# Performance work log

Hardware: AMD Instinct MI355X
Metric: run time of the kernel (lower is better)

Reference implementation:

```python
import jax, jax.numpy as jnp
import numpy as np

POPULATION = 1000000.0  # __init__ arg of MarkovChainRNN_Model
B, T, F = 16384, 2048, 2  # batch, timesteps, (beta, gamma) per step


def setup_inputs() -> dict:
    key = jax.random.key(0)
    k1, k2 = jax.random.split(key)
    # per-step (beta, gamma) rates in [0, 1)
    inputs = jax.random.uniform(k1, (B, T, F), dtype=jnp.float32)
    # initial [S, I, R] state; scaled so S+I+R is O(population)
    initial_state = jax.random.uniform(k2, (B, 3), dtype=jnp.float32) * POPULATION
    return {"inputs": inputs, "initial_state": initial_state}


def reference(inputs, initial_state):
    # SIR cell update, one step per day:
    #   new_inf = beta * S * I / N ; new_rec = gamma * I
    #   S' = S - new_inf ; I' = I + new_inf - new_rec ; R' = R + new_rec
    # Keras RNN(cell, return_state=True) -> (last_output, last_state);
    # for an SIR cell output == state, so both returns are the final state.
    def step(state, u):
        beta, gamma = u[:, 0], u[:, 1]            # [B], [B]
        S, I, R = state[:, 0], state[:, 1], state[:, 2]
        new_inf = beta * S * I / POPULATION
        new_rec = gamma * I
        new_state = jnp.stack([S - new_inf,
                               I + new_inf - new_rec,
                               R + new_rec], axis=-1)  # [B, 3]
        return new_state, None

    xs = jnp.transpose(inputs, (1, 0, 2))  # time-major [T, B, F]
    final_state, _ = jax.lax.scan(step, initial_state, xs)
    return (final_state, final_state)
```

## Files before the change

### kernel.cpp

```cpp
#include <hip/hip_runtime.h>
#include <stdint.h>
#include <stddef.h>
#include <math.h>


#define T_STEPS 2048
#define C_STEPS 64
#define NCHUNK  (T_STEPS / C_STEPS)
#define BPB     64
#define PAIRS   (C_STEPS / 2)
#define IPC     32

#define INV_POP 1e-6f

__device__ __forceinline__ void stage_chunk(const float* __restrict__ in,
                                            float4* lds, int b0, int c, int lane)
{
    const int hi = lane >> 5;
    const int q  = lane & 31;
#pragma unroll
    for (int j = 0; j < IPC; ++j) {
        const int bi = 2 * j + hi;
        const int p  = q ^ (bi & 15);
        const float* g = in
            + (size_t)(b0 + bi) * (T_STEPS * 2)
            + (size_t)c * (C_STEPS * 2)
            + (size_t)(p * 4);
        float4* l = lds + j * 64;
        __builtin_amdgcn_global_load_lds(
            (__attribute__((address_space(1))) void*)g,
            (__attribute__((address_space(3))) void*)l,
            16, 0, 0);
    }
}

__device__ __forceinline__ void compute_chunk(const float4* lds, int tid,
                                              float& S, float& I, float& rsum)
{
    const int swz = tid & 15;
    const float4* row = lds + tid * PAIRS;
#pragma unroll
    for (int p = 0; p < PAIRS; ++p) {
        const float4 v = row[p ^ swz];

        float u  = v.x * INV_POP;
        float t1 = u * S;
        float t2 = u * I;
        float w  = fmaf(-v.y, I, I);
        rsum     = fmaf(v.y, I, rsum);
        I = fmaf(I, t1, w);
        S = fmaf(-t2, S, S);

        u  = v.z * INV_POP;
        t1 = u * S;
        t2 = u * I;
        w  = fmaf(-v.w, I, I);
        rsum = fmaf(v.w, I, rsum);
        I = fmaf(I, t1, w);
        S = fmaf(-t2, S, S);
    }
}

#define BAR()    asm volatile("s_barrier" ::: "memory")
#define WAIT32() asm volatile("s_waitcnt vmcnt(32)" ::: "memory")
#define WAIT0()  asm volatile("s_waitcnt vmcnt(0)"  ::: "memory")

__global__ __launch_bounds__(128)
void sir_scan_kernel(const float* __restrict__ in, const float* __restrict__ init,
                     float* __restrict__ out, int half)
{
    __shared__ float4 buf0[BPB * PAIRS];
    __shared__ float4 buf1[BPB * PAIRS];
    __shared__ float4 buf2[BPB * PAIRS];
    __shared__ float4 buf3[BPB * PAIRS];

    const int tid = threadIdx.x;
    const int b0  = blockIdx.x * BPB;

    if (tid < 64) {
        const int gb = b0 + tid;
        float S  = init[gb * 3 + 0];
        float I  = init[gb * 3 + 1];
        float R0 = init[gb * 3 + 2];
        float rsum = 0.0f;

#pragma unroll 1
        for (int c = 0; c < NCHUNK; c += 4) {
            BAR(); compute_chunk(buf0, tid, S, I, rsum);
            BAR(); compute_chunk(buf1, tid, S, I, rsum);
            BAR(); compute_chunk(buf2, tid, S, I, rsum);
            BAR(); compute_chunk(buf3, tid, S, I, rsum);
        }

        const float R = R0 + rsum;
        out[gb * 3 + 0] = S;
        out[gb * 3 + 1] = I;
        out[gb * 3 + 2] = R;
        out[half + gb * 3 + 0] = S;
        out[half + gb * 3 + 1] = I;
        out[half + gb * 3 + 2] = R;
    } else {
        const int lane = tid - 64;

        stage_chunk(in, buf0, b0, 0, lane);
        stage_chunk(in, buf1, b0, 1, lane);

#pragma unroll 1
        for (int c = 0; c < NCHUNK - 4; c += 4) {
            WAIT32(); BAR(); stage_chunk(in, buf2, b0, c + 2, lane);
            WAIT32(); BAR(); stage_chunk(in, buf3, b0, c + 3, lane);
            WAIT32(); BAR(); stage_chunk(in, buf0, b0, c + 4, lane);
            WAIT32(); BAR(); stage_chunk(in, buf1, b0, c + 5, lane);
        }
        WAIT32(); BAR(); stage_chunk(in, buf2, b0, NCHUNK - 2, lane);
        WAIT32(); BAR(); stage_chunk(in, buf3, b0, NCHUNK - 1, lane);
        WAIT32(); BAR();
        WAIT0();  BAR();
    }
}

extern "C" void kernel_launch(void* const* d_in, const int* in_sizes, int n_in,
                              void* d_out, int out_size, void* d_ws, size_t ws_size,
                              hipStream_t stream) {
    (void)in_sizes; (void)n_in; (void)d_ws; (void)ws_size;
    const float* in   = (const float*)d_in[0];
    const float* init = (const float*)d_in[1];
    float* out        = (float*)d_out;
    const int half = out_size / 2;

    dim3 grid(16384 / BPB);
    dim3 block(128);
    sir_scan_kernel<<<grid, block, 0, stream>>>(in, init, out, half);
}
```

Before: 58.51 us.

## Replace producer/consumer warp split with single-wave register double-buffered pipeline

Each block now holds one 64-lane wave that serves 16 batch rows. The wave loads chunks into registers (two buffers), writes them to a small swizzled LDS tile, and computes from it, with 4 lanes redundantly running each row's recurrence. This drops the separate loader wave, the s_barrier handshakes and the global_load_lds path, and raises block count from 256 to 1024 to spread work across more CUs. The cost is 4x redundant compute per row, register pressure from 16 float4 staging registers, and reliance on wave-level lockstep instead of barriers when the single LDS tile is reused.

```diff
diff --git a/kernel.cpp b/kernel.cpp
--- a/kernel.cpp
+++ b/kernel.cpp
@@ -7,91 +7,106 @@
 #define T_STEPS 2048
 #define C_STEPS 64
 #define NCHUNK  (T_STEPS / C_STEPS)
-#define BPB     64
-#define PAIRS   (C_STEPS / 2)
-#define IPC     32
+#define BPW     16
+#define SLOTS   (C_STEPS / 2)
+#define LPC     8
 
 #define INV_POP 1e-6f
 
-__device__ __forceinline__ void stage_chunk(const float* __restrict__ in,
-                                            float4* lds, int b0, int c, int lane)
+__device__ __forceinline__ void load_chunk(const float* __restrict__ in,
+                                           int b0, int c, int lane, float4* r)
 {
     const int hi = lane >> 5;
-    const int q  = lane & 31;
+    const int s  = lane & 31;
 #pragma unroll
-    for (int j = 0; j < IPC; ++j) {
-        const int bi = 2 * j + hi;
-        const int p  = q ^ (bi & 15);
+    for (int j = 0; j < LPC; ++j) {
         const float* g = in
-            + (size_t)(b0 + bi) * (T_STEPS * 2)
+            + (size_t)(b0 + 2 * j + hi) * (T_STEPS * 2)
             + (size_t)c * (C_STEPS * 2)
-            + (size_t)(p * 4);
-        float4* l = lds + j * 64;
-        __builtin_amdgcn_global_load_lds(
-            (__attribute__((address_space(1))) void*)g,
-            (__attribute__((address_space(3))) void*)l,
-            16, 0, 0);
+            + (size_t)(s * 4);
+        r[j] = *(const float4*)g;
     }
 }
 
-__device__ __forceinline__ void compute_chunk(const float4* lds, int tid,
-                                              float& S, float& I, float& rsum)
+__device__ __forceinline__ void write_chunk(float4* lds, int lane,
+                                            const float4* r)
 {
-    const int swz = tid & 15;
-    const float4* row = lds + tid * PAIRS;
+    const int hi = lane >> 5;
+    const int s  = lane & 31;
 #pragma unroll
-    for (int p = 0; p < PAIRS; ++p) {
-        const float4 v = row[p ^ swz];
-
-        float u  = v.x * INV_POP;
-        float t1 = u * S;
-        float t2 = u * I;
-        float w  = fmaf(-v.y, I, I);
-        rsum     = fmaf(v.y, I, rsum);
-        I = fmaf(I, t1, w);
-        S = fmaf(-t2, S, S);
-
-        u  = v.z * INV_POP;
-        t1 = u * S;
-        t2 = u * I;
-        w  = fmaf(-v.w, I, I);
-        rsum = fmaf(v.w, I, rsum);
-        I = fmaf(I, t1, w);
-        S = fmaf(-t2, S, S);
+    for (int j = 0; j < LPC; ++j) {
+        const int row = 2 * j + hi;
+        lds[row * SLOTS + (s ^ (row & 7))] = r[j];
     }
 }
 
-#define BAR()    asm volatile("s_barrier" ::: "memory")
-#define WAIT32() asm volatile("s_waitcnt vmcnt(32)" ::: "memory")
-#define WAIT0()  asm volatile("s_waitcnt vmcnt(0)"  ::: "memory")
+__device__ __forceinline__ void compute_chunk(const float4* lds, int rr,
+                                              float& S, float& I, float& rsum)
+{
+    const int swz = rr & 7;
+    const float4* row = lds + rr * SLOTS;
+#pragma unroll 1
+    for (int g = 0; g < SLOTS / 4; ++g) {
+#pragma unroll
+        for (int k = 0; k < 4; ++k) {
+            const int s = g * 4 + k;
+            const float4 v = row[s ^ swz];
 
-__global__ __launch_bounds__(128)
+            float u  = v.x * INV_POP;
+            float t1 = u * S;
+            float t2 = u * I;
+            float w  = fmaf(-v.y, I, I);
+            rsum     = fmaf(v.y, I, rsum);
+            I = fmaf(I, t1, w);
+            S = fmaf(-t2, S, S);
+
+            u  = v.z * INV_POP;
+            t1 = u * S;
+            t2 = u * I;
+            w  = fmaf(-v.w, I, I);
+            rsum = fmaf(v.w, I, rsum);
+            I = fmaf(I, t1, w);
+            S = fmaf(-t2, S, S);
+        }
+    }
+}
+
+#define LGKM0() asm volatile("s_waitcnt lgkmcnt(0)" ::: "memory")
+
+__global__ __launch_bounds__(64)
 void sir_scan_kernel(const float* __restrict__ in, const float* __restrict__ init,
                      float* __restrict__ out, int half)
 {
-    __shared__ float4 buf0[BPB * PAIRS];
-    __shared__ float4 buf1[BPB * PAIRS];
-    __shared__ float4 buf2[BPB * PAIRS];
-    __shared__ float4 buf3[BPB * PAIRS];
+    __shared__ float4 lds[BPW * SLOTS];
 
     const int tid = threadIdx.x;
-    const int b0  = blockIdx.x * BPB;
+    const int b0  = blockIdx.x * BPW;
+    const int rr  = tid & 15;
+    const int gb  = b0 + rr;
 
-    if (tid < 64) {
-        const int gb = b0 + tid;
-        float S  = init[gb * 3 + 0];
-        float I  = init[gb * 3 + 1];
-        float R0 = init[gb * 3 + 2];
-        float rsum = 0.0f;
+    float S  = init[gb * 3 + 0];
+    float I  = init[gb * 3 + 1];
+    float R0 = init[gb * 3 + 2];
+    float rsum = 0.0f;
+
+    float4 rA[LPC], rB[LPC];
+    load_chunk(in, b0, 0, tid, rA);
+    load_chunk(in, b0, 1, tid, rB);
 
 #pragma unroll 1
-        for (int c = 0; c < NCHUNK; c += 4) {
-            BAR(); compute_chunk(buf0, tid, S, I, rsum);
-            BAR(); compute_chunk(buf1, tid, S, I, rsum);
-            BAR(); compute_chunk(buf2, tid, S, I, rsum);
-            BAR(); compute_chunk(buf3, tid, S, I, rsum);
-        }
+    for (int c = 0; c < NCHUNK; c += 2) {
+        write_chunk(lds, tid, rA);
+        LGKM0();
+        if (c + 2 < NCHUNK) load_chunk(in, b0, c + 2, tid, rA);
+        compute_chunk(lds, rr, S, I, rsum);
 
+        write_chunk(lds, tid, rB);
+        LGKM0();
+        if (c + 3 < NCHUNK) load_chunk(in, b0, c + 3, tid, rB);
+        compute_chunk(lds, rr, S, I, rsum);
+    }
+
+    if (tid < BPW) {
         const float R = R0 + rsum;
         out[gb * 3 + 0] = S;
         out[gb * 3 + 1] = I;
@@ -99,23 +114,6 @@
         out[half + gb * 3 + 0] = S;
         out[half + gb * 3 + 1] = I;
         out[half + gb * 3 + 2] = R;
-    } else {
-        const int lane = tid - 64;
-
-        stage_chunk(in, buf0, b0, 0, lane);
-        stage_chunk(in, buf1, b0, 1, lane);
-
-#pragma unroll 1
-        for (int c = 0; c < NCHUNK - 4; c += 4) {
-            WAIT32(); BAR(); stage_chunk(in, buf2, b0, c + 2, lane);
-            WAIT32(); BAR(); stage_chunk(in, buf3, b0, c + 3, lane);
-            WAIT32(); BAR(); stage_chunk(in, buf0, b0, c + 4, lane);
-            WAIT32(); BAR(); stage_chunk(in, buf1, b0, c + 5, lane);
-        }
-        WAIT32(); BAR(); stage_chunk(in, buf2, b0, NCHUNK - 2, lane);
-        WAIT32(); BAR(); stage_chunk(in, buf3, b0, NCHUNK - 1, lane);
-        WAIT32(); BAR();
-        WAIT0();  BAR();
     }
 }
 
@@ -128,7 +126,7 @@
     float* out        = (float*)d_out;
     const int half = out_size / 2;
 
-    dim3 grid(16384 / BPB);
-    dim3 block(128);
+    dim3 grid(16384 / BPW);
+    dim3 block(64);
     sir_scan_kernel<<<grid, block, 0, stream>>>(in, init, out, half);
 }
```

Measured after the change: 122.3 us. 109% more time.
